# Performance work log

Measured on AMD Instinct MI355X. Metric: run time of the kernel, lower is better.

The kernel has to match this reference:

```python
import jax, jax.numpy as jnp
import numpy as np

L, H, P = 32768, 512, 256


def setup_inputs() -> dict:
    key = jax.random.key(0)
    ks = jax.random.split(key, 9)
    sH = 1.0 / np.sqrt(H).astype(np.float32)
    sP = 1.0 / np.sqrt(P).astype(np.float32)
    return {
        "input_sequence": jax.random.normal(ks[0], (L, H), jnp.float32),
        "Lambda_re": jax.random.normal(ks[1], (P,), jnp.float32),
        "Lambda_im": jax.random.normal(ks[2], (P,), jnp.float32) * np.float32(np.pi),
        "B_re": jax.random.normal(ks[3], (P, H), jnp.float32) * sH,
        "B_im": jax.random.normal(ks[4], (P, H), jnp.float32) * sH,
        "C_re": jax.random.normal(ks[5], (H, P), jnp.float32) * sP,
        "C_im": jax.random.normal(ks[6], (H, P), jnp.float32) * sP,
        "D": jax.random.normal(ks[7], (H,), jnp.float32),
        "log_step": jax.random.normal(ks[8], (P,), jnp.float32) - 3.0,
    }


def reference(input_sequence, Lambda_re, Lambda_im, B_re, B_im, C_re, C_im, D, log_step):
    # clip_eigs=True: enforce left-half-plane eigenvalues
    Lambda = jnp.clip(Lambda_re, None, -1e-4) + 1j * Lambda_im          # (P,)
    B_tilde = B_re + 1j * B_im                                          # (P,H)
    C_tilde = C_re + 1j * C_im                                          # (H,P)
    step = jnp.exp(log_step)                                            # step_rescale = 1.0, (P,)

    # ZOH discretization
    Lambda_bar = jnp.exp(Lambda * step)                                 # (P,) complex64
    B_bar = ((Lambda_bar - 1.0) / Lambda)[:, None] * B_tilde            # (P,H) complex64

    # Bu_elements: (L,P) complex; equivalent to vmap(lambda u: B_bar @ u)
    Bu = input_sequence.astype(B_bar.dtype) @ B_bar.T                   # (L,P)
    Lambda_elems = jnp.broadcast_to(Lambda_bar, (input_sequence.shape[0], Lambda_bar.shape[0]))

    def binop(q_i, q_j):
        A_i, b_i = q_i
        A_j, b_j = q_j
        return A_j * A_i, A_j * b_i + b_j

    _, xs = jax.lax.associative_scan(binop, (Lambda_elems, Bu))         # xs: (L,P)

    # conj_sym=True: ys = 2 * Re(C_tilde @ x) per step
    ys = 2.0 * (xs @ C_tilde.T).real                                    # (L,H)
    return ys + D * input_sequence
```

## Files before the change

### kernel.cpp

```cpp
#include <hip/hip_runtime.h>
#include <cstdint>
#include <cstddef>

typedef __bf16 bf16x8 __attribute__((ext_vector_type(8)));
typedef __bf16 bf16x2 __attribute__((ext_vector_type(2)));
typedef float f32x4 __attribute__((ext_vector_type(4)));

#define L_SEQ 32768
#define H_DIM 512
#define P_DIM 256
#define NP2   512
#define CHUNK 32
#define NCHUNK 1024
#define NSUPER 32

__device__ __forceinline__ void gload_lds16(const void* g, void* l) {
    __builtin_amdgcn_global_load_lds(
        (const __attribute__((address_space(1))) void*)g,
        (__attribute__((address_space(3))) void*)l,
        16, 0, 0);
}

__global__ void setup_kernel(const float* __restrict__ Lre, const float* __restrict__ Lim,
                             const float* __restrict__ lstep,
                             const float* __restrict__ Bre, const float* __restrict__ Bim,
                             const float* __restrict__ Cre, const float* __restrict__ Cim,
                             const float4* __restrict__ uin,
                             float* __restrict__ par,
                             __bf16* __restrict__ Bt, __bf16* __restrict__ Ct,
                             bf16x8* __restrict__ Ubf) {
    int b = blockIdx.x;
    if (b == 0) {
        int p = threadIdx.x;
        float lr = fminf(Lre[p], -1e-4f);
        float li = Lim[p];
        float st = expf(lstep[p]);
        float ldr = lr * st;
        float ldi = li * st;
        float er = expf(ldr);
        par[p]        = er * cosf(ldi);
        par[256 + p]  = er * sinf(ldi);
        float e32  = expf((float)CHUNK * ldr);
        float ph32 = (float)CHUNK * ldi;
        par[1024 + p] = e32 * cosf(ph32);
        par[1280 + p] = e32 * sinf(ph32);
        par[1536 + p] = ldr;
        par[1792 + p] = ldi;
    } else if (b <= 1024) {
        int bb = b - 1;
        if (bb < 512) {
            int idx = bb * 256 + threadIdx.x;
            int p = idx >> 9;
            float lr = fminf(Lre[p], -1e-4f);
            float li = Lim[p];
            float st = expf(lstep[p]);
            float er = expf(lr * st);
            float ar = er * cosf(li * st);
            float ai = er * sinf(li * st);
            float den = lr * lr + li * li;
            float mr = ar - 1.0f, mi = ai;
            float cr = (mr * lr + mi * li) / den;
            float ci = (mi * lr - mr * li) / den;
            float br = Bre[idx], bi = Bim[idx];
            int h = idx & 511;
            Bt[(size_t)p * NP2 + h]         = (__bf16)(cr * br - ci * bi);
            Bt[(size_t)(256 + p) * NP2 + h] = (__bf16)(cr * bi + ci * br);
        } else {
            int idx = (bb - 512) * 256 + threadIdx.x;
            int h = idx >> 8;
            int q = idx & 255;
            Ct[(size_t)h * NP2 + q]       = (__bf16)( 2.0f * Cre[idx]);
            Ct[(size_t)h * NP2 + 256 + q] = (__bf16)(-2.0f * Cim[idx]);
        }
    } else {
        int i = (b - 1025) * 256 + threadIdx.x;
        float4 a = uin[2 * i], c = uin[2 * i + 1];
        bf16x8 v;
        v[0] = (__bf16)a.x; v[1] = (__bf16)a.y; v[2] = (__bf16)a.z; v[3] = (__bf16)a.w;
        v[4] = (__bf16)c.x; v[5] = (__bf16)c.y; v[6] = (__bf16)c.z; v[7] = (__bf16)c.w;
        Ubf[i] = v;
    }
}

template<bool FUSE>
__global__ __launch_bounds__(256)
void gemm_bt_kernel(const __bf16* __restrict__ A, const __bf16* __restrict__ Bt,
                    void* __restrict__ CoutV, const float* __restrict__ Dvec,
                    const __bf16* __restrict__ Ubf) {
    const int K = NP2, N = NP2;
    __shared__ __align__(16) __bf16 As[3][128 * 64];
    __shared__ __align__(16) __bf16 Bs[2][128 * 64];
    const int t = threadIdx.x;
    const int l = t & 63;
    const int w = t >> 6;
    const int wr = w >> 1, wc = w & 1;
    const int b    = blockIdx.x;
    const int n_sw = (b & 7) * 128 + (b >> 3);
    const int row0 = (n_sw >> 2) * 128;
    const int col0 = (n_sw & 3) * 128;
    const int lr = l & 15;
    const int lk = (l >> 4) * 8;
    f32x4 acc[4][4] = {};

    auto STAGE_A = [&](int buf, int k0) {
#pragma unroll
        for (int i = 0; i < 4; ++i) {
            int off = i * 256 + t;
            int r  = off >> 3;
            int ce = ((off & 7) ^ (r & 7)) * 8;
            gload_lds16(A + (size_t)(row0 + r) * K + (k0 + ce), &As[buf][off * 8]);
        }
    };
    auto STAGE_B = [&](int buf, int k0) {
#pragma unroll
        for (int i = 0; i < 4; ++i) {
            int off = i * 256 + t;
            int r  = off >> 3;
            int ce = ((off & 7) ^ (r & 7)) * 8;
            gload_lds16(Bt + (size_t)(col0 + r) * K + (k0 + ce), &Bs[buf][off * 8]);
        }
    };

    auto COMPUTE = [&](int ba, int bb) {
#pragma unroll
        for (int kk = 0; kk < 64; kk += 32) {
            bf16x8 a[4], b2[4];
            const int ls = (kk + lk) >> 3;
#pragma unroll
            for (int m = 0; m < 4; ++m) {
                int row = wr * 64 + m * 16 + lr;
                a[m] = *reinterpret_cast<const bf16x8*>(&As[ba][row * 64 + ((ls ^ (row & 7)) << 3)]);
            }
#pragma unroll
            for (int n = 0; n < 4; ++n) {
                int row = wc * 64 + n * 16 + lr;
                b2[n] = *reinterpret_cast<const bf16x8*>(&Bs[bb][row * 64 + ((ls ^ (row & 7)) << 3)]);
            }
            __builtin_amdgcn_s_setprio(1);
#pragma unroll
            for (int m = 0; m < 4; ++m)
#pragma unroll
                for (int n = 0; n < 4; ++n)
                    acc[m][n] = __builtin_amdgcn_mfma_f32_16x16x32_bf16(a[m], b2[n], acc[m][n], 0, 0, 0);
            __builtin_amdgcn_s_setprio(0);
        }
    };

    STAGE_A(0, 0);
    STAGE_B(0, 0);
    STAGE_A(1, 64);
#pragma unroll
    for (int ks = 0; ks < 8; ++ks) {
        if (ks + 1 < 8) STAGE_B((ks + 1) & 1, (ks + 1) * 64);
        if (ks + 2 < 8) STAGE_A((ks + 2) % 3, (ks + 2) * 64);
        if (ks <= 5)      { asm volatile("s_waitcnt vmcnt(12)" ::: "memory"); }
        else if (ks == 6) { asm volatile("s_waitcnt vmcnt(8)"  ::: "memory"); }
        else              { asm volatile("s_waitcnt vmcnt(0)"  ::: "memory"); }
        __builtin_amdgcn_s_barrier();
        __builtin_amdgcn_sched_barrier(0);
        COMPUTE(ks % 3, ks & 1);
        __builtin_amdgcn_sched_barrier(0);
        __builtin_amdgcn_s_barrier();
    }

    const int lg = (l >> 4) * 4;
#pragma unroll
    for (int m = 0; m < 4; ++m) {
#pragma unroll
        for (int n = 0; n < 4; ++n) {
            int col = col0 + wc * 64 + n * 16 + lr;
#pragma unroll
            for (int j = 0; j < 4; ++j) {
                int row = row0 + wr * 64 + m * 16 + lg + j;
                size_t o = (size_t)row * N + col;
                if (FUSE) {
                    ((float*)CoutV)[o] = acc[m][n][j] + Dvec[col] * (float)Ubf[o];
                } else {
                    ((__bf16*)CoutV)[o] = (__bf16)acc[m][n][j];
                }
            }
        }
    }
}

__global__ void scanA_kernel(const __bf16* __restrict__ Bu, const float* __restrict__ par,
                             float4* __restrict__ Fc) {
    int g = blockIdx.x;
    int t = threadIdx.x;
    int p0 = 2 * t;
    float ar0 = par[p0], ai0 = par[256 + p0];
    float ar1 = par[p0 + 1], ai1 = par[256 + p0 + 1];
    const __bf16* bu = Bu + (size_t)g * CHUNK * NP2;
    float xr0 = 0.f, xi0 = 0.f, xr1 = 0.f, xi1 = 0.f;
#pragma unroll 4
    for (int i = 0; i < CHUNK; ++i) {
        bf16x2 re = *reinterpret_cast<const bf16x2*>(bu + i * NP2 + p0);
        bf16x2 im = *reinterpret_cast<const bf16x2*>(bu + i * NP2 + 256 + p0);
        float nr0 = fmaf(ar0, xr0, fmaf(-ai0, xi0, (float)re[0]));
        float ni0 = fmaf(ar0, xi0, fmaf( ai0, xr0, (float)im[0]));
        float nr1 = fmaf(ar1, xr1, fmaf(-ai1, xi1, (float)re[1]));
        float ni1 = fmaf(ar1, xi1, fmaf( ai1, xr1, (float)im[1]));
        xr0 = nr0; xi0 = ni0; xr1 = nr1; xi1 = ni1;
    }
    float4 f; f.x = xr0; f.y = xi0; f.z = xr1; f.w = xi1;
    Fc[g * 128 + t] = f;
}

__global__ void scanB1_kernel(const float4* __restrict__ Fc, const float* __restrict__ par,
                              float4* __restrict__ Lc, float4* __restrict__ Tc) {
    int s = blockIdx.x;
    int t = threadIdx.x;
    int p0 = 2 * t;
    float pr0 = par[1024 + p0], pi0 = par[1280 + p0];
    float pr1 = par[1024 + p0 + 1], pi1 = par[1280 + p0 + 1];
    float er0 = 0.f, ei0 = 0.f, er1 = 0.f, ei1 = 0.f;
    int base = s * 32;
#pragma unroll
    for (int j = 0; j < 32; ++j) {
        float4 e; e.x = er0; e.y = ei0; e.z = er1; e.w = ei1;
        Lc[(base + j) * 128 + t] = e;
        float4 f = Fc[(base + j) * 128 + t];
        float nr0 = fmaf(pr0, er0, fmaf(-pi0, ei0, f.x));
        float ni0 = fmaf(pr0, ei0, fmaf( pi0, er0, f.y));
        float nr1 = fmaf(pr1, er1, fmaf(-pi1, ei1, f.z));
        float ni1 = fmaf(pr1, ei1, fmaf( pi1, er1, f.w));
        er0 = nr0; ei0 = ni0; er1 = nr1; ei1 = ni1;
    }
    float4 tt; tt.x = er0; tt.y = ei0; tt.z = er1; tt.w = ei1;
    Tc[s * 128 + t] = tt;
}

__global__ void scanC_kernel(const __bf16* __restrict__ Bu, const float* __restrict__ par,
                             const float4* __restrict__ Lc, const float4* __restrict__ Tc,
                             __bf16* __restrict__ xs) {
    int g = blockIdx.x;
    int t = threadIdx.x;
    int s = g >> 5, k = g & 31;
    int p0 = 2 * t;
    float ar0 = par[p0], ai0 = par[256 + p0];
    float ar1 = par[p0 + 1], ai1 = par[256 + p0 + 1];
    float ldr0 = par[1536 + p0], ldi0 = par[1792 + p0];
    float ldr1 = par[1536 + p0 + 1], ldi1 = par[1792 + p0 + 1];
    float e10 = expf(1024.0f * ldr0), ph10 = 1024.0f * ldi0;
    float q1r0 = e10 * cosf(ph10), q1i0 = e10 * sinf(ph10);
    float e11 = expf(1024.0f * ldr1), ph11 = 1024.0f * ldi1;
    float q1r1 = e11 * cosf(ph11), q1i1 = e11 * sinf(ph11);
    float er0 = 0.f, ei0 = 0.f, er1 = 0.f, ei1 = 0.f;
    for (int s2 = 0; s2 < s; ++s2) {
        float4 f = Tc[s2 * 128 + t];
        float nr0 = fmaf(q1r0, er0, fmaf(-q1i0, ei0, f.x));
        float ni0 = fmaf(q1r0, ei0, fmaf( q1i0, er0, f.y));
        float nr1 = fmaf(q1r1, er1, fmaf(-q1i1, ei1, f.z));
        float ni1 = fmaf(q1r1, ei1, fmaf( q1i1, er1, f.w));
        er0 = nr0; ei0 = ni0; er1 = nr1; ei1 = ni1;
    }
    float kk = (float)(32 * k);
    float ek0 = expf(kk * ldr0), phk0 = kk * ldi0;
    float qr0 = ek0 * cosf(phk0), qi0 = ek0 * sinf(phk0);
    float ek1 = expf(kk * ldr1), phk1 = kk * ldi1;
    float qr1 = ek1 * cosf(phk1), qi1 = ek1 * sinf(phk1);
    float4 l0 = Lc[g * 128 + t];
    float xr0 = fmaf(qr0, er0, fmaf(-qi0, ei0, l0.x));
    float xi0 = fmaf(qr0, ei0, fmaf( qi0, er0, l0.y));
    float xr1 = fmaf(qr1, er1, fmaf(-qi1, ei1, l0.z));
    float xi1 = fmaf(qr1, ei1, fmaf( qi1, er1, l0.w));
    const __bf16* bu = Bu + (size_t)g * CHUNK * NP2;
    __bf16* xo = xs + (size_t)g * CHUNK * NP2;
#pragma unroll 4
    for (int i = 0; i < CHUNK; ++i) {
        bf16x2 re = *reinterpret_cast<const bf16x2*>(bu + i * NP2 + p0);
        bf16x2 im = *reinterpret_cast<const bf16x2*>(bu + i * NP2 + 256 + p0);
        float nr0 = fmaf(ar0, xr0, fmaf(-ai0, xi0, (float)re[0]));
        float ni0 = fmaf(ar0, xi0, fmaf( ai0, xr0, (float)im[0]));
        float nr1 = fmaf(ar1, xr1, fmaf(-ai1, xi1, (float)re[1]));
        float ni1 = fmaf(ar1, xi1, fmaf( ai1, xr1, (float)im[1]));
        xr0 = nr0; xi0 = ni0; xr1 = nr1; xi1 = ni1;
        bf16x2 wre; wre[0] = (__bf16)xr0; wre[1] = (__bf16)xr1;
        bf16x2 wim; wim[0] = (__bf16)xi0; wim[1] = (__bf16)xi1;
        *reinterpret_cast<bf16x2*>(xo + i * NP2 + p0)       = wre;
        *reinterpret_cast<bf16x2*>(xo + i * NP2 + 256 + p0) = wim;
    }
}

extern "C" void kernel_launch(void* const* d_in, const int* in_sizes, int n_in,
                              void* d_out, int out_size, void* d_ws, size_t ws_size,
                              hipStream_t stream) {
    const float* u   = (const float*)d_in[0];
    const float* Lre = (const float*)d_in[1];
    const float* Lim = (const float*)d_in[2];
    const float* Bre = (const float*)d_in[3];
    const float* Bim = (const float*)d_in[4];
    const float* Cre = (const float*)d_in[5];
    const float* Cim = (const float*)d_in[6];
    const float* Dv  = (const float*)d_in[7];
    const float* lst = (const float*)d_in[8];

    char* w = (char*)d_ws;
    size_t off = 0;
    float* par = (float*)(w + off);      off += 16 * 1024;
    __bf16* Btm = (__bf16*)(w + off);    off += (size_t)NP2 * NP2 * 2;
    __bf16* Ctm = (__bf16*)(w + off);    off += (size_t)NP2 * NP2 * 2;
    float4* Fc = (float4*)(w + off);     off += (size_t)NCHUNK * 128 * 16;
    float4* Lc = (float4*)(w + off);     off += (size_t)NCHUNK * 128 * 16;
    float4* Tc = (float4*)(w + off);     off += (size_t)NSUPER * 128 * 16;
    __bf16* Ubf = (__bf16*)(w + off);    off += (size_t)L_SEQ * H_DIM * 2;
    __bf16* Xs  = (__bf16*)(w + off);    off += (size_t)L_SEQ * NP2 * 2;
    if (ws_size < off) return;

    __bf16* Bu = (__bf16*)d_out;

    setup_kernel  <<<9217, 256, 0, stream>>>(Lre, Lim, lst, Bre, Bim, Cre, Cim,
                                             (const float4*)u, par, Btm, Ctm, (bf16x8*)Ubf);
    gemm_bt_kernel<false><<<1024, 256, 0, stream>>>(Ubf, Btm, (void*)Bu, nullptr, nullptr);
    scanA_kernel  <<<NCHUNK, 128, 0, stream>>>(Bu, par, Fc);
    scanB1_kernel <<<NSUPER, 128, 0, stream>>>(Fc, par, Lc, Tc);
    scanC_kernel  <<<NCHUNK, 128, 0, stream>>>(Bu, par, Lc, Tc, Xs);
    gemm_bt_kernel<true><<<1024, 256, 0, stream>>>(Xs, Ctm, d_out, Dv, Ubf);
}
```

Measured before the change: 98.36 us.

## Enlarge GEMM tiles to 256x256 with 8 waves and interleaved half-K pipelining

Both GEMMs now use 256x256 output tiles computed by 512-thread blocks (8 waves, each owning 128x64), launched as 256 blocks instead of 1024. K is staged in 32-wide halves, double-buffered, with global-to-LDS loads for the next tile issued between MFMA groups and a new XOR swizzle. The aim is more operand reuse per LDS byte and fewer global reloads of A/B. In exchange, 256 blocks only about fill the CUs once, accumulator registers double (acc[8][4]), and the finer barrier schedule may stall.

```diff
diff --git a/kernel.cpp b/kernel.cpp
--- a/kernel.cpp
+++ b/kernel.cpp
@@ -83,95 +83,141 @@
 }
 
 template<bool FUSE>
-__global__ __launch_bounds__(256)
+__global__ __launch_bounds__(512, 2)
 void gemm_bt_kernel(const __bf16* __restrict__ A, const __bf16* __restrict__ Bt,
                     void* __restrict__ CoutV, const float* __restrict__ Dvec,
                     const __bf16* __restrict__ Ubf) {
     const int K = NP2, N = NP2;
-    __shared__ __align__(16) __bf16 As[3][128 * 64];
-    __shared__ __align__(16) __bf16 Bs[2][128 * 64];
+    __shared__ __align__(16) __bf16 As[2][2][256 * 32];
+    __shared__ __align__(16) __bf16 Bs[2][2][256 * 32];
     const int t = threadIdx.x;
     const int l = t & 63;
     const int w = t >> 6;
-    const int wr = w >> 1, wc = w & 1;
+    const int wr = w >> 2;
+    const int wc = w & 3;
     const int b    = blockIdx.x;
-    const int n_sw = (b & 7) * 128 + (b >> 3);
-    const int row0 = (n_sw >> 2) * 128;
-    const int col0 = (n_sw & 3) * 128;
+    const int n_sw = (b & 7) * 32 + (b >> 3);
+    const int row0 = (n_sw >> 1) * 256;
+    const int col0 = (n_sw & 1) * 256;
     const int lr = l & 15;
-    const int lk = (l >> 4) * 8;
-    f32x4 acc[4][4] = {};
-
-    auto STAGE_A = [&](int buf, int k0) {
-#pragma unroll
-        for (int i = 0; i < 4; ++i) {
-            int off = i * 256 + t;
-            int r  = off >> 3;
-            int ce = ((off & 7) ^ (r & 7)) * 8;
-            gload_lds16(A + (size_t)(row0 + r) * K + (k0 + ce), &As[buf][off * 8]);
-        }
-    };
-    auto STAGE_B = [&](int buf, int k0) {
-#pragma unroll
-        for (int i = 0; i < 4; ++i) {
-            int off = i * 256 + t;
-            int r  = off >> 3;
-            int ce = ((off & 7) ^ (r & 7)) * 8;
-            gload_lds16(Bt + (size_t)(col0 + r) * K + (k0 + ce), &Bs[buf][off * 8]);
-        }
-    };
-
-    auto COMPUTE = [&](int ba, int bb) {
-#pragma unroll
-        for (int kk = 0; kk < 64; kk += 32) {
-            bf16x8 a[4], b2[4];
-            const int ls = (kk + lk) >> 3;
-#pragma unroll
-            for (int m = 0; m < 4; ++m) {
-                int row = wr * 64 + m * 16 + lr;
-                a[m] = *reinterpret_cast<const bf16x8*>(&As[ba][row * 64 + ((ls ^ (row & 7)) << 3)]);
-            }
-#pragma unroll
-            for (int n = 0; n < 4; ++n) {
-                int row = wc * 64 + n * 16 + lr;
-                b2[n] = *reinterpret_cast<const bf16x8*>(&Bs[bb][row * 64 + ((ls ^ (row & 7)) << 3)]);
-            }
-            __builtin_amdgcn_s_setprio(1);
-#pragma unroll
-            for (int m = 0; m < 4; ++m)
-#pragma unroll
-                for (int n = 0; n < 4; ++n)
-                    acc[m][n] = __builtin_amdgcn_mfma_f32_16x16x32_bf16(a[m], b2[n], acc[m][n], 0, 0, 0);
-            __builtin_amdgcn_s_setprio(0);
-        }
-    };
-
-    STAGE_A(0, 0);
-    STAGE_B(0, 0);
-    STAGE_A(1, 64);
-#pragma unroll
-    for (int ks = 0; ks < 8; ++ks) {
-        if (ks + 1 < 8) STAGE_B((ks + 1) & 1, (ks + 1) * 64);
-        if (ks + 2 < 8) STAGE_A((ks + 2) % 3, (ks + 2) * 64);
-        if (ks <= 5)      { asm volatile("s_waitcnt vmcnt(12)" ::: "memory"); }
-        else if (ks == 6) { asm volatile("s_waitcnt vmcnt(8)"  ::: "memory"); }
-        else              { asm volatile("s_waitcnt vmcnt(0)"  ::: "memory"); }
-        __builtin_amdgcn_s_barrier();
-        __builtin_amdgcn_sched_barrier(0);
-        COMPUTE(ks % 3, ks & 1);
+    const int lk = l >> 4;
+    f32x4 acc[8][4] = {};
+
+    auto STAGE_A = [&](int tt, int h) {
+        const int k0 = tt * 64 + h * 32;
+        __bf16* dst = &As[tt & 1][h][0];
+#pragma unroll
+        for (int i = 0; i < 2; ++i) {
+            int off = i * 512 + t;
+            int r  = off >> 2;
+            int sl = off & 3;
+            int ce = k0 + ((sl ^ ((r >> 2) & 3)) << 3);
+            gload_lds16(A + (size_t)(row0 + r) * K + ce, dst + off * 8);
+        }
+    };
+    auto STAGE_B = [&](int tt, int h) {
+        const int k0 = tt * 64 + h * 32;
+        __bf16* dst = &Bs[tt & 1][h][0];
+#pragma unroll
+        for (int i = 0; i < 2; ++i) {
+            int off = i * 512 + t;
+            int r  = off >> 2;
+            int sl = off & 3;
+            int ce = k0 + ((sl ^ ((r >> 2) & 3)) << 3);
+            gload_lds16(Bt + (size_t)(col0 + r) * K + ce, dst + off * 8);
+        }
+    };
+
+    auto RD_A = [&](int s, int h, int m) -> bf16x8 {
+        int row = wr * 128 + m * 16 + lr;
+        return *reinterpret_cast<const bf16x8*>(
+            &As[s][h][row * 32 + ((lk ^ ((row >> 2) & 3)) << 3)]);
+    };
+    auto RD_B = [&](int s, int h, int n) -> bf16x8 {
+        int row = wc * 64 + n * 16 + lr;
+        return *reinterpret_cast<const bf16x8*>(
+            &Bs[s][h][row * 32 + ((lk ^ ((row >> 2) & 3)) << 3)]);
+    };
+
+    auto MFMA16 = [&](bf16x8 (&a)[4], bf16x8 (&b2)[4], int mlo) {
+        __builtin_amdgcn_s_setprio(1);
+#pragma unroll
+        for (int m = 0; m < 4; ++m)
+#pragma unroll
+            for (int n = 0; n < 4; ++n)
+                acc[mlo + m][n] = __builtin_amdgcn_mfma_f32_16x16x32_bf16(
+                    a[m], b2[n], acc[mlo + m][n], 0, 0, 0);
+        __builtin_amdgcn_s_setprio(0);
+    };
+
+    STAGE_A(0, 0); STAGE_B(0, 0);
+    STAGE_A(0, 1); STAGE_B(0, 1);
+    asm volatile("s_waitcnt vmcnt(4)" ::: "memory");
+    __builtin_amdgcn_s_barrier();
+
+#pragma unroll
+    for (int tt = 0; tt < 8; ++tt) {
+        const int s = tt & 1;
+        bf16x8 a[4], b2[4];
+#pragma unroll
+        for (int n = 0; n < 4; ++n) b2[n] = RD_B(s, 0, n);
+#pragma unroll
+        for (int m = 0; m < 4; ++m) a[m] = RD_A(s, 0, m);
+        __builtin_amdgcn_sched_barrier(0);
+        if (tt < 7) STAGE_A(tt + 1, 0);
+        __builtin_amdgcn_s_barrier();
+        __builtin_amdgcn_sched_barrier(0);
+        MFMA16(a, b2, 0);
+        __builtin_amdgcn_sched_barrier(0);
+        __builtin_amdgcn_s_barrier();
+#pragma unroll
+        for (int m = 0; m < 4; ++m) a[m] = RD_A(s, 0, 4 + m);
+        __builtin_amdgcn_sched_barrier(0);
+        if (tt < 7) {
+            STAGE_B(tt + 1, 0);
+            asm volatile("s_waitcnt vmcnt(4)" ::: "memory");
+        } else {
+            asm volatile("s_waitcnt vmcnt(0)" ::: "memory");
+        }
+        __builtin_amdgcn_s_barrier();
+        __builtin_amdgcn_sched_barrier(0);
+        MFMA16(a, b2, 4);
+        __builtin_amdgcn_sched_barrier(0);
+        __builtin_amdgcn_s_barrier();
+#pragma unroll
+        for (int n = 0; n < 4; ++n) b2[n] = RD_B(s, 1, n);
+#pragma unroll
+        for (int m = 0; m < 4; ++m) a[m] = RD_A(s, 1, m);
+        __builtin_amdgcn_sched_barrier(0);
+        if (tt < 7) STAGE_A(tt + 1, 1);
+        __builtin_amdgcn_s_barrier();
+        __builtin_amdgcn_sched_barrier(0);
+        MFMA16(a, b2, 0);
+        __builtin_amdgcn_sched_barrier(0);
+        __builtin_amdgcn_s_barrier();
+#pragma unroll
+        for (int m = 0; m < 4; ++m) a[m] = RD_A(s, 1, 4 + m);
+        __builtin_amdgcn_sched_barrier(0);
+        if (tt < 7) {
+            STAGE_B(tt + 1, 1);
+            asm volatile("s_waitcnt vmcnt(4)" ::: "memory");
+        }
+        __builtin_amdgcn_s_barrier();
+        __builtin_amdgcn_sched_barrier(0);
+        MFMA16(a, b2, 4);
         __builtin_amdgcn_sched_barrier(0);
         __builtin_amdgcn_s_barrier();
     }
 
     const int lg = (l >> 4) * 4;
 #pragma unroll
-    for (int m = 0; m < 4; ++m) {
+    for (int m = 0; m < 8; ++m) {
 #pragma unroll
         for (int n = 0; n < 4; ++n) {
             int col = col0 + wc * 64 + n * 16 + lr;
 #pragma unroll
             for (int j = 0; j < 4; ++j) {
-                int row = row0 + wr * 64 + m * 16 + lg + j;
+                int row = row0 + wr * 128 + m * 16 + lg + j;
                 size_t o = (size_t)row * N + col;
                 if (FUSE) {
                     ((float*)CoutV)[o] = acc[m][n][j] + Dvec[col] * (float)Ubf[o];
@@ -311,9 +357,9 @@
 
     setup_kernel  <<<9217, 256, 0, stream>>>(Lre, Lim, lst, Bre, Bim, Cre, Cim,
                                              (const float4*)u, par, Btm, Ctm, (bf16x8*)Ubf);
-    gemm_bt_kernel<false><<<1024, 256, 0, stream>>>(Ubf, Btm, (void*)Bu, nullptr, nullptr);
+    gemm_bt_kernel<false><<<256, 512, 0, stream>>>(Ubf, Btm, (void*)Bu, nullptr, nullptr);
     scanA_kernel  <<<NCHUNK, 128, 0, stream>>>(Bu, par, Fc);
     scanB1_kernel <<<NSUPER, 128, 0, stream>>>(Fc, par, Lc, Tc);
     scanC_kernel  <<<NCHUNK, 128, 0, stream>>>(Bu, par, Lc, Tc, Xs);
-    gemm_bt_kernel<true><<<1024, 256, 0, stream>>>(Xs, Ctm, d_out, Dv, Ubf);
-}
+    gemm_bt_kernel<true><<<256, 512, 0, stream>>>(Xs, Ctm, d_out, Dv, Ubf);
+}
```

Result: slower. 101.6 us (+3.3%).

## Keep full B panel in LDS and stream A fragments directly from global

Applied to the files above, without the earlier changes.

The GEMM kernel now loads the whole 128x512 B panel (128 KB) into LDS once per block and reads A fragments straight from global memory into registers with register double-buffering. This removes the per-k-step LDS staging barriers for A. Blocks grow to 512 threads covering a 256-row tile, so the grid halves. The large LDS footprint limits occupancy to one block per CU, despite the launch bound asking for two. Uncoalesced A loads from global could also add latency that nothing hides.

```diff
diff --git a/kernel.cpp b/kernel.cpp
--- a/kernel.cpp
+++ b/kernel.cpp
@@ -83,84 +83,69 @@
 }
 
 template<bool FUSE>
-__global__ __launch_bounds__(256)
+__global__ __launch_bounds__(512, 2)
 void gemm_bt_kernel(const __bf16* __restrict__ A, const __bf16* __restrict__ Bt,
                     void* __restrict__ CoutV, const float* __restrict__ Dvec,
                     const __bf16* __restrict__ Ubf) {
     const int K = NP2, N = NP2;
-    __shared__ __align__(16) __bf16 As[3][128 * 64];
-    __shared__ __align__(16) __bf16 Bs[2][128 * 64];
+    __shared__ __align__(16) __bf16 Bs[128 * 512];
     const int t = threadIdx.x;
     const int l = t & 63;
     const int w = t >> 6;
-    const int wr = w >> 1, wc = w & 1;
+    const int wr = w >> 1;
+    const int wc = w & 1;
     const int b    = blockIdx.x;
-    const int n_sw = (b & 7) * 128 + (b >> 3);
-    const int row0 = (n_sw >> 2) * 128;
+    const int n_sw = (b & 7) * 64 + (b >> 3);
+    const int row0 = (n_sw >> 2) * 256;
     const int col0 = (n_sw & 3) * 128;
     const int lr = l & 15;
     const int lk = (l >> 4) * 8;
+
+#pragma unroll
+    for (int i = 0; i < 16; ++i) {
+        int chunk = i * 512 + t;
+        int r = chunk >> 6;
+        int s = chunk & 63;
+        gload_lds16(Bt + (size_t)(col0 + r) * K + ((s ^ (r & 7)) << 3),
+                    Bs + chunk * 8);
+    }
+    asm volatile("s_waitcnt vmcnt(0)" ::: "memory");
+    __builtin_amdgcn_s_barrier();
+
     f32x4 acc[4][4] = {};
-
-    auto STAGE_A = [&](int buf, int k0) {
-#pragma unroll
-        for (int i = 0; i < 4; ++i) {
-            int off = i * 256 + t;
-            int r  = off >> 3;
-            int ce = ((off & 7) ^ (r & 7)) * 8;
-            gload_lds16(A + (size_t)(row0 + r) * K + (k0 + ce), &As[buf][off * 8]);
-        }
+    bf16x8 a[2][8];
+    auto LOADA = [&](int buf, int tt) {
+#pragma unroll
+        for (int kk2 = 0; kk2 < 2; ++kk2)
+#pragma unroll
+            for (int m = 0; m < 4; ++m)
+                a[buf][kk2 * 4 + m] = *reinterpret_cast<const bf16x8*>(
+                    A + (size_t)(row0 + wr * 64 + m * 16 + lr) * K
+                      + tt * 64 + kk2 * 32 + lk);
     };
-    auto STAGE_B = [&](int buf, int k0) {
-#pragma unroll
-        for (int i = 0; i < 4; ++i) {
-            int off = i * 256 + t;
-            int r  = off >> 3;
-            int ce = ((off & 7) ^ (r & 7)) * 8;
-            gload_lds16(Bt + (size_t)(col0 + r) * K + (k0 + ce), &Bs[buf][off * 8]);
-        }
-    };
-
-    auto COMPUTE = [&](int ba, int bb) {
-#pragma unroll
-        for (int kk = 0; kk < 64; kk += 32) {
-            bf16x8 a[4], b2[4];
-            const int ls = (kk + lk) >> 3;
-#pragma unroll
-            for (int m = 0; m < 4; ++m) {
-                int row = wr * 64 + m * 16 + lr;
-                a[m] = *reinterpret_cast<const bf16x8*>(&As[ba][row * 64 + ((ls ^ (row & 7)) << 3)]);
-            }
+
+    LOADA(0, 0);
+#pragma unroll
+    for (int tt = 0; tt < 8; ++tt) {
+        const int cur = tt & 1;
+        if (tt < 7) LOADA(cur ^ 1, tt + 1);
+#pragma unroll
+        for (int kk2 = 0; kk2 < 2; ++kk2) {
+            bf16x8 b2[4];
 #pragma unroll
             for (int n = 0; n < 4; ++n) {
                 int row = wc * 64 + n * 16 + lr;
-                b2[n] = *reinterpret_cast<const bf16x8*>(&Bs[bb][row * 64 + ((ls ^ (row & 7)) << 3)]);
+                int sl  = tt * 8 + kk2 * 4 + (l >> 4);
+                b2[n] = *reinterpret_cast<const bf16x8*>(
+                    &Bs[row * 512 + ((sl ^ (row & 7)) << 3)]);
             }
-            __builtin_amdgcn_s_setprio(1);
 #pragma unroll
             for (int m = 0; m < 4; ++m)
 #pragma unroll
                 for (int n = 0; n < 4; ++n)
-                    acc[m][n] = __builtin_amdgcn_mfma_f32_16x16x32_bf16(a[m], b2[n], acc[m][n], 0, 0, 0);
-            __builtin_amdgcn_s_setprio(0);
+                    acc[m][n] = __builtin_amdgcn_mfma_f32_16x16x32_bf16(
+                        a[cur][kk2 * 4 + m], b2[n], acc[m][n], 0, 0, 0);
         }
-    };
-
-    STAGE_A(0, 0);
-    STAGE_B(0, 0);
-    STAGE_A(1, 64);
-#pragma unroll
-    for (int ks = 0; ks < 8; ++ks) {
-        if (ks + 1 < 8) STAGE_B((ks + 1) & 1, (ks + 1) * 64);
-        if (ks + 2 < 8) STAGE_A((ks + 2) % 3, (ks + 2) * 64);
-        if (ks <= 5)      { asm volatile("s_waitcnt vmcnt(12)" ::: "memory"); }
-        else if (ks == 6) { asm volatile("s_waitcnt vmcnt(8)"  ::: "memory"); }
-        else              { asm volatile("s_waitcnt vmcnt(0)"  ::: "memory"); }
-        __builtin_amdgcn_s_barrier();
-        __builtin_amdgcn_sched_barrier(0);
-        COMPUTE(ks % 3, ks & 1);
-        __builtin_amdgcn_sched_barrier(0);
-        __builtin_amdgcn_s_barrier();
     }
 
     const int lg = (l >> 4) * 4;
@@ -311,9 +296,9 @@
 
     setup_kernel  <<<9217, 256, 0, stream>>>(Lre, Lim, lst, Bre, Bim, Cre, Cim,
                                              (const float4*)u, par, Btm, Ctm, (bf16x8*)Ubf);
-    gemm_bt_kernel<false><<<1024, 256, 0, stream>>>(Ubf, Btm, (void*)Bu, nullptr, nullptr);
+    gemm_bt_kernel<false><<<512, 512, 0, stream>>>(Ubf, Btm, (void*)Bu, nullptr, nullptr);
     scanA_kernel  <<<NCHUNK, 128, 0, stream>>>(Bu, par, Fc);
     scanB1_kernel <<<NSUPER, 128, 0, stream>>>(Fc, par, Lc, Tc);
     scanC_kernel  <<<NCHUNK, 128, 0, stream>>>(Bu, par, Lc, Tc, Xs);
-    gemm_bt_kernel<true><<<1024, 256, 0, stream>>>(Xs, Ctm, d_out, Dv, Ubf);
-}
+    gemm_bt_kernel<true><<<512, 512, 0, stream>>>(Xs, Ctm, d_out, Dv, Ubf);
+}
```

New measurement: 130.8 us. 1.33x slower.
